# Kernel tuning notes

Hardware: AMD Instinct MI355X
Metric: run time of the kernel (lower is better)

Reference implementation:

```python
import jax, jax.numpy as jnp
import numpy as np

MIN_STD = 0.1  # cfg.min_std_dev
B, T1, S, A, H, E = 256, 128, 128, 32, 1024, 1024  # batch, T-1, state, action, belief=hidden, embedding


def setup_inputs() -> dict:
    key = jax.random.key(0)
    ks = jax.random.split(key, 16)
    f32 = jnp.float32
    def p(k, shape, fan):
        return jax.random.normal(k, shape, f32) / np.float32(np.sqrt(fan))
    return {
        "s_0": jax.random.normal(ks[0], (B, S), f32),
        "b_0": jax.random.normal(ks[1], (B, H), f32),
        "Action": jax.random.normal(ks[2], (B, T1, A), f32),
        "Observation": jax.random.normal(ks[3], (B, T1, E), f32),
        "noise_pri": jax.random.normal(ks[4], (B, T1, S), f32),
        "noise_pos": jax.random.normal(ks[5], (B, T1, S), f32),
        "W_sa": p(ks[6], (H, S + A), S + A), "b_sa": jnp.zeros((H,), f32),
        "W_ih": p(ks[7], (3 * H, H), H), "W_hh": p(ks[8], (3 * H, H), H),
        "b_ih": jnp.zeros((3 * H,), f32), "b_hh": jnp.zeros((3 * H,), f32),
        "W_bpri": p(ks[9], (H, H), H), "b_bpri": jnp.zeros((H,), f32),
        "W_spri": p(ks[10], (2 * S, H), H), "b_spri": jnp.zeros((2 * S,), f32),
        "W_bpos": p(ks[11], (H, H + E), H + E), "b_bpos": jnp.zeros((H,), f32),
        "W_spos": p(ks[12], (2 * S, H), H), "b_spos": jnp.zeros((2 * S,), f32),
    }


def reference(s_0, b_0, Action, Observation, noise_pri, noise_pos,
              W_sa, b_sa, W_ih, W_hh, b_ih, b_hh,
              W_bpri, b_bpri, W_spri, b_spri,
              W_bpos, b_bpos, W_spos, b_spos):
    act = jax.nn.relu  # cfg.activation_function = 'relu'

    def gru(x, h):  # torch.nn.GRUCell semantics, gate order r,z,n
        gi = x @ W_ih.T + b_ih
        gh = h @ W_hh.T + b_hh
        ir, iz, in_ = jnp.split(gi, 3, axis=1)
        hr, hz, hn = jnp.split(gh, 3, axis=1)
        r = jax.nn.sigmoid(ir + hr)
        z = jax.nn.sigmoid(iz + hz)
        n = jnp.tanh(in_ + r * hn)
        return (1.0 - z) * n + z * h

    def step(carry, inp):
        b, s = carry  # belief, posterior state (Observation is provided)
        a, o, ep, eq = inp
        x = act(jnp.concatenate([s, a], axis=1) @ W_sa.T + b_sa)
        b1 = gru(x, b)
        # prior
        hp = act(b1 @ W_bpri.T + b_bpri)
        mu_p, hp2 = jnp.split(hp @ W_spri.T + b_spri, 2, axis=1)
        std_p = jax.nn.softplus(hp2) + MIN_STD
        s_p = mu_p + std_p * ep
        # posterior (uses Observation[:, t])
        hq = act(jnp.concatenate([b1, o], axis=1) @ W_bpos.T + b_bpos)
        mu_q, hq2 = jnp.split(hq @ W_spos.T + b_spos, 2, axis=1)
        std_q = jax.nn.softplus(hq2) + MIN_STD
        s_q = mu_q + std_q * eq
        return (b1, s_q), (b1, s_p, mu_p, std_p, s_q, mu_q, std_q)

    xs = (jnp.swapaxes(Action, 0, 1), jnp.swapaxes(Observation, 0, 1),
          jnp.swapaxes(noise_pri, 0, 1), jnp.swapaxes(noise_pos, 0, 1))
    _, ys = jax.lax.scan(step, (b_0, s_0), xs)
    # time-major [T-1, B, D] -> batch-major [B, T-1, D]
    return tuple(jnp.swapaxes(y, 0, 1) for y in ys)
```

## Files before the change

### kernel.cpp

```cpp
#include <hip/hip_runtime.h>
#include <hip/hip_bf16.h>

typedef __hip_bfloat16 bf16;
using bf16x8 = __attribute__((ext_vector_type(8))) short;
using f32x4  = __attribute__((ext_vector_type(4))) float;

#define B_   256
#define T1_  128
#define S_   128
#define A_   32
#define H_   1024
#define E_   1024
#define MIN_STD 0.1f

__device__ __forceinline__ float loadT(const void* p, int isbf, long idx) {
  return isbf ? __bfloat162float(((const bf16*)p)[idx]) : ((const float*)p)[idx];
}
__device__ __forceinline__ void storeT(void* p, int isbf, long idx, float v) {
  if (isbf) ((bf16*)p)[idx] = __float2bfloat16(v);
  else      ((float*)p)[idx] = v;
}

__global__ void dtype_probe(const void* __restrict__ p, int nelem, int* __restrict__ flag) {
  __shared__ int bad;
  if (threadIdx.x == 0) bad = 0;
  __syncthreads();
  const bf16* q = (const bf16*)p;
  int lbad = 0;
  for (int i = threadIdx.x; i < nelem; i += 256) {
    float v = __bfloat162float(q[i]);
    if (!(fabsf(v) <= 1e6f)) lbad = 1;
  }
  if (lbad) atomicOr(&bad, 1);
  __syncthreads();
  if (threadIdx.x == 0) *flag = bad ? 0 : 1;
}

__global__ __launch_bounds__(256)
void split_plane(const void* __restrict__ src, long n, bf16* __restrict__ h,
                 bf16* __restrict__ l, const int* __restrict__ flagp) {
  const int F = *flagp;
  long i = (long)blockIdx.x * 256 + threadIdx.x;
  if (i < n) {
    float v = loadT(src, F, i);
    bf16 hv = __float2bfloat16(v);
    h[i] = hv;
    l[i] = __float2bfloat16(v - __bfloat162float(hv));
  }
}

struct GProb {
  const bf16 *Ah, *Al; int lda;
  const bf16 *A2h, *A2l; int lda2; int K1; long aoff2;
  const bf16 *Wh, *Wl; int ldw;
  const void* bias;
  float* Cf; bf16 *Ch, *Cl; int ldc;
  int relu; int nbx; int K;
};

__device__ __forceinline__ void gemm_seg(f32x4 (&acc)[2][2],
    const bf16* __restrict__ ah, const bf16* __restrict__ al, int lda, long abase,
    int ks, int ke,
    const bf16* __restrict__ wh, const bf16* __restrict__ wl, int ldw,
    int r0, int c0, int lk)
{
  #pragma unroll 2
  for (int kt = ks; kt < ke; kt += 32) {
    bf16x8 fa_h[2], fa_l[2], fw_h[2], fw_l[2];
    #pragma unroll
    for (int i = 0; i < 2; ++i) {
      long ao = (long)(r0 + i * 16) * lda + abase + (kt - ks) + lk;
      fa_h[i] = *(const bf16x8*)(ah + ao);
      fa_l[i] = *(const bf16x8*)(al + ao);
      long wo = (long)(c0 + i * 16) * ldw + kt + lk;
      fw_h[i] = *(const bf16x8*)(wh + wo);
      fw_l[i] = *(const bf16x8*)(wl + wo);
    }
    #pragma unroll
    for (int i = 0; i < 2; ++i)
      #pragma unroll
      for (int j = 0; j < 2; ++j) {
        acc[i][j] = __builtin_amdgcn_mfma_f32_16x16x32_bf16(fa_h[i], fw_h[j], acc[i][j], 0, 0, 0);
        acc[i][j] = __builtin_amdgcn_mfma_f32_16x16x32_bf16(fa_l[i], fw_h[j], acc[i][j], 0, 0, 0);
        acc[i][j] = __builtin_amdgcn_mfma_f32_16x16x32_bf16(fa_h[i], fw_l[j], acc[i][j], 0, 0, 0);
      }
  }
}

__global__ __launch_bounds__(256)
void mfma_gemm(GProb p0, GProb p1, GProb p2, int n0, int n01,
               const int* __restrict__ flagp)
{
  int blk = blockIdx.x;
  GProb p;
  if (blk < n0) p = p0;
  else if (blk < n01) { blk -= n0; p = p1; }
  else { blk -= n01; p = p2; }
  const int F = *flagp;

  const int bx   = blk % p.nbx;
  const int by   = blk / p.nbx;
  const int m0   = by * 64;
  const int nc0  = bx * 64;
  const int w    = threadIdx.x >> 6;
  const int lane = threadIdx.x & 63;
  const int wm   = (w >> 1) * 32;
  const int wn   = (w & 1) * 32;
  const int lr   = lane & 15;
  const int lk   = (lane >> 4) * 8;

  const int r0 = m0 + wm + lr;
  const int c0 = nc0 + wn + lr;

  f32x4 zz = {0.f, 0.f, 0.f, 0.f};
  f32x4 acc[2][2] = {{zz, zz}, {zz, zz}};

  gemm_seg(acc, p.Ah, p.Al, p.lda, 0, 0, p.K1, p.Wh, p.Wl, p.ldw, r0, c0, lk);
  if (p.K1 < p.K)
    gemm_seg(acc, p.A2h, p.A2l, p.lda2, p.aoff2, p.K1, p.K, p.Wh, p.Wl, p.ldw, r0, c0, lk);

  float bv0 = loadT(p.bias, F, c0);
  float bv1 = loadT(p.bias, F, c0 + 16);
  const int rb = m0 + wm + ((lane >> 4) << 2);
  #pragma unroll
  for (int i = 0; i < 2; ++i) {
    #pragma unroll
    for (int j = 0; j < 2; ++j) {
      const int n  = c0 + j * 16;
      const float bv = j ? bv1 : bv0;
      #pragma unroll
      for (int r = 0; r < 4; ++r) {
        float v = acc[i][j][r] + bv;
        if (p.relu) v = fmaxf(v, 0.f);
        long o = (long)(rb + i * 16 + r) * p.ldc + n;
        if (p.Cf) p.Cf[o] = v;
        if (p.Ch) {
          bf16 hv = __float2bfloat16(v);
          p.Ch[o] = hv;
          p.Cl[o] = __float2bfloat16(v - __bfloat162float(hv));
        }
      }
    }
  }
}

__global__ __launch_bounds__(256)
void gru_ew(const float* __restrict__ gi, const float* __restrict__ gh,
            const void* __restrict__ hprev, int hm,
            void* __restrict__ out, int t, float* __restrict__ b_f,
            bf16* __restrict__ bh, bf16* __restrict__ bl,
            const void* __restrict__ Obs, bf16* __restrict__ oh,
            bf16* __restrict__ ol, const int* __restrict__ flagp)
{
  const int F = *flagp;
  const int fh = hm & F;
  int tid = blockIdx.x * 256 + threadIdx.x;
  int b = tid >> 10;
  int j = tid & 1023;
  long gbase = (long)b * 3072;
  float ir  = gi[gbase + j],        hr = gh[gbase + j];
  float iz  = gi[gbase + 1024 + j], hz = gh[gbase + 1024 + j];
  float in_ = gi[gbase + 2048 + j], hn = gh[gbase + 2048 + j];
  float h = loadT(hprev, fh, (long)b * H_ + j);
  float r = 1.f / (1.f + expf(-(ir + hr)));
  float z = 1.f / (1.f + expf(-(iz + hz)));
  float n = tanhf(in_ + r * hn);
  float v = (1.f - z) * n + z * h;
  storeT(out, F, (long)b * (T1_ * H_) + (long)t * H_ + j, v);
  b_f[tid] = v;
  bf16 vh = __float2bfloat16(v);
  bh[tid] = vh;
  bl[tid] = __float2bfloat16(v - __bfloat162float(vh));
  float ov = loadT(Obs, F, (long)b * (T1_ * E_) + (long)t * E_ + j);
  bf16 ovh = __float2bfloat16(ov);
  oh[tid] = ovh;
  ol[tid] = __float2bfloat16(ov - __bfloat162float(ovh));
}

__device__ __forceinline__ float softplusf_(float x) {
  return fmaxf(x, 0.f) + log1pf(expf(-fabsf(x)));
}

__global__ __launch_bounds__(256)
void sample_ew(const float* __restrict__ catp, const float* __restrict__ catq,
               const void* __restrict__ npri, const void* __restrict__ npos,
               void* __restrict__ out, int t,
               bf16* __restrict__ sh, bf16* __restrict__ sl,
               const int* __restrict__ flagp)
{
  const int F = *flagp;
  int tid = blockIdx.x * 256 + threadIdx.x;
  int b = tid >> 7;
  int s = tid & 127;
  const long SZH = (long)B_ * T1_ * H_;
  const long SZS = (long)B_ * T1_ * S_;
  long nidx = (long)b * (T1_ * S_) + (long)t * S_ + s;
  long crow = (long)b * 256;
  float mu_p = catp[crow + s];
  float h2p  = catp[crow + 128 + s];
  float mu_q = catq[crow + s];
  float h2q  = catq[crow + 128 + s];
  float std_p = softplusf_(h2p) + MIN_STD;
  float std_q = softplusf_(h2q) + MIN_STD;
  float s_p = mu_p + std_p * loadT(npri, F, nidx);
  float s_q = mu_q + std_q * loadT(npos, F, nidx);
  storeT(out, F, SZH + 0 * SZS + nidx, s_p);
  storeT(out, F, SZH + 1 * SZS + nidx, mu_p);
  storeT(out, F, SZH + 2 * SZS + nidx, std_p);
  storeT(out, F, SZH + 3 * SZS + nidx, s_q);
  storeT(out, F, SZH + 4 * SZS + nidx, mu_q);
  storeT(out, F, SZH + 5 * SZS + nidx, std_q);
  bf16 qh = __float2bfloat16(s_q);
  sh[tid] = qh;
  sl[tid] = __float2bfloat16(s_q - __bfloat162float(qh));
}

extern "C" void kernel_launch(void* const* d_in, const int* in_sizes, int n_in,
                              void* d_out, int out_size, void* d_ws, size_t ws_size,
                              hipStream_t stream) {
  const void* s0     = d_in[0];
  const void* b0     = d_in[1];
  const void* Act    = d_in[2];
  const void* Obs    = d_in[3];
  const void* npri   = d_in[4];
  const void* npos   = d_in[5];
  const void* W_sa   = d_in[6];
  const void* b_sa   = d_in[7];
  const void* W_ih   = d_in[8];
  const void* W_hh   = d_in[9];
  const void* b_ih   = d_in[10];
  const void* b_hh   = d_in[11];
  const void* W_bpri = d_in[12];
  const void* b_bpri = d_in[13];
  const void* W_spri = d_in[14];
  const void* b_spri = d_in[15];
  const void* W_bpos = d_in[16];
  const void* b_bpos = d_in[17];
  const void* W_spos = d_in[18];
  const void* b_spos = d_in[19];
  (void)in_sizes; (void)n_in; (void)out_size; (void)ws_size;

  char* base = (char*)d_ws;
  size_t off = 0;
  auto carve = [&](size_t bytes) {
    void* p = base + off;
    off = (off + bytes + 255) & ~(size_t)255;
    return p;
  };
  float* gi_f   = (float*)carve(sizeof(float) * B_ * 3 * H_);
  float* gh_f   = (float*)carve(sizeof(float) * B_ * 3 * H_);
  float* b_f    = (float*)carve(sizeof(float) * B_ * H_);
  float* catp_f = (float*)carve(sizeof(float) * B_ * 2 * S_);
  float* catq_f = (float*)carve(sizeof(float) * B_ * 2 * S_);
  int*   flagp  = (int*)carve(256);
  auto plane = [&](size_t n) { return (bf16*)carve(2 * n); };
  bf16 *xh = plane((size_t)B_ * H_),  *xl = plane((size_t)B_ * H_);
  bf16 *bh = plane((size_t)B_ * H_),  *bl = plane((size_t)B_ * H_);
  bf16 *hph = plane((size_t)B_ * H_), *hpl = plane((size_t)B_ * H_);
  bf16 *hqh = plane((size_t)B_ * H_), *hql = plane((size_t)B_ * H_);
  bf16 *sh = plane((size_t)B_ * S_),  *sl = plane((size_t)B_ * S_);
  bf16 *oh = plane((size_t)B_ * E_),  *ol = plane((size_t)B_ * E_);
  bf16 *acth = plane((size_t)B_ * T1_ * A_), *actl = plane((size_t)B_ * T1_ * A_);
  bf16 *wsah  = plane((size_t)H_ * (S_ + A_)), *wsal  = plane((size_t)H_ * (S_ + A_));
  bf16 *wihh  = plane((size_t)3 * H_ * H_),    *wihl  = plane((size_t)3 * H_ * H_);
  bf16 *whhh  = plane((size_t)3 * H_ * H_),    *whhl  = plane((size_t)3 * H_ * H_);
  bf16 *wprih = plane((size_t)H_ * H_),        *wpril = plane((size_t)H_ * H_);
  bf16 *wsprih = plane((size_t)2 * S_ * H_),   *wspril = plane((size_t)2 * S_ * H_);
  bf16 *wposh = plane((size_t)H_ * (H_ + E_)), *wposl = plane((size_t)H_ * (H_ + E_));
  bf16 *wsposh = plane((size_t)2 * S_ * H_),   *wsposl = plane((size_t)2 * S_ * H_);

  dim3 blk(256);

  dtype_probe<<<dim3(1), blk, 0, stream>>>(W_ih, 8192, flagp);
  auto split = [&](const void* src, size_t n, bf16* h, bf16* l) {
    split_plane<<<dim3((unsigned)((n + 255) / 256)), blk, 0, stream>>>(src, (long)n, h, l, flagp);
  };
  split(W_sa,   (size_t)H_ * (S_ + A_), wsah, wsal);
  split(W_ih,   (size_t)3 * H_ * H_,    wihh, wihl);
  split(W_hh,   (size_t)3 * H_ * H_,    whhh, whhl);
  split(W_bpri, (size_t)H_ * H_,        wprih, wpril);
  split(W_spri, (size_t)2 * S_ * H_,    wsprih, wspril);
  split(W_bpos, (size_t)H_ * (H_ + E_), wposh, wposl);
  split(W_spos, (size_t)2 * S_ * H_,    wsposh, wsposl);
  split(s0,  (size_t)B_ * S_,        sh, sl);
  split(b0,  (size_t)B_ * H_,        bh, bl);
  split(Act, (size_t)B_ * T1_ * A_,  acth, actl);

  auto mk = [](const bf16* Ah, const bf16* Al, int lda,
               const bf16* A2h, const bf16* A2l, int lda2, int K1, long aoff2,
               const bf16* Wh, const bf16* Wl, int ldw, const void* bias,
               float* Cf, bf16* Ch, bf16* Cl, int ldc, int relu, int N, int K) {
    GProb p;
    p.Ah = Ah; p.Al = Al; p.lda = lda;
    p.A2h = A2h; p.A2l = A2l; p.lda2 = lda2; p.K1 = K1; p.aoff2 = aoff2;
    p.Wh = Wh; p.Wl = Wl; p.ldw = ldw; p.bias = bias;
    p.Cf = Cf; p.Ch = Ch; p.Cl = Cl; p.ldc = ldc;
    p.relu = relu; p.nbx = N / 64; p.K = K;
    return p;
  };

  GProb Pgh = mk(bh, bl, H_,  bh, bl, H_, H_, 0,  whhh, whhl, H_, b_hh,
                 gh_f, nullptr, nullptr, 3 * H_, 0, 3 * H_, H_);
  GProb Pgi = mk(xh, xl, H_,  xh, xl, H_, H_, 0,  wihh, wihl, H_, b_ih,
                 gi_f, nullptr, nullptr, 3 * H_, 0, 3 * H_, H_);
  GProb Px  = mk(sh, sl, S_,  acth, actl, T1_ * A_, S_, 0, wsah, wsal, S_ + A_, b_sa,
                 nullptr, xh, xl, H_, 1, H_, S_ + A_);
  GProb Php = mk(bh, bl, H_,  bh, bl, H_, H_, 0,  wprih, wpril, H_, b_bpri,
                 nullptr, hph, hpl, H_, 1, H_, H_);
  GProb Phq = mk(bh, bl, H_,  oh, ol, E_, H_, 0,  wposh, wposl, H_ + E_, b_bpos,
                 nullptr, hqh, hql, H_, 1, H_, H_ + E_);
  GProb Pcp = mk(hph, hpl, H_, hph, hpl, H_, H_, 0, wsprih, wspril, H_, b_spri,
                 catp_f, nullptr, nullptr, 2 * S_, 0, 2 * S_, H_);
  GProb Pcq = mk(hqh, hql, H_, hqh, hql, H_, H_, 0, wsposh, wsposl, H_, b_spos,
                 catq_f, nullptr, nullptr, 2 * S_, 0, 2 * S_, H_);

  mfma_gemm<<<dim3(192), blk, 0, stream>>>(Pgh, Pgh, Pgh, 192, 192, flagp);

  for (int t = 0; t < T1_; ++t) {
    Px.aoff2 = (long)t * A_;
    mfma_gemm<<<dim3(64), blk, 0, stream>>>(Px, Px, Px, 64, 64, flagp);
    mfma_gemm<<<dim3(192), blk, 0, stream>>>(Pgi, Pgi, Pgi, 192, 192, flagp);
    gru_ew<<<dim3(B_ * H_ / 256), blk, 0, stream>>>(
        gi_f, gh_f, t ? (const void*)b_f : b0, t ? 0 : 1,
        d_out, t, b_f, bh, bl, Obs, oh, ol, flagp);
    mfma_gemm<<<dim3(64 + 64 + 192), blk, 0, stream>>>(Php, Phq, Pgh, 64, 128, flagp);
    mfma_gemm<<<dim3(32), blk, 0, stream>>>(Pcp, Pcq, Pcq, 16, 32, flagp);
    sample_ew<<<dim3(B_ * S_ / 256), blk, 0, stream>>>(
        catp_f, catq_f, npri, npos, d_out, t, sh, sl, flagp);
  }
}
```

Measured before the change: 21.27 ms.

## Fuse recurrent time loop into one persistent kernel with grid barriers

Replaces the per-timestep sequence of six kernel launches with a single persistent 256-block kernel that walks all timesteps, separating phases with a custom atomic grid barrier. GEMM tiles grow from 64x64 to 128x128 per block. The observation half of the posterior GEMM is computed off the critical path, alongside the input-gate GEMM. The posterior sample is rebuilt inside the x-projection tile instead of being staged through bf16 planes. This removes roughly 768 launches and their gaps, at the cost of fewer active blocks per GEMM and a grid barrier that deadlocks unless all 256 blocks are co-resident.

```diff
diff --git a/kernel.cpp b/kernel.cpp
--- a/kernel.cpp
+++ b/kernel.cpp
@@ -12,6 +12,8 @@
 #define H_   1024
 #define E_   1024
 #define MIN_STD 0.1f
+#define GRID_ 256
+#define ASTRIDE 16
 
 __device__ __forceinline__ float loadT(const void* p, int isbf, long idx) {
   return isbf ? __bfloat162float(((const bf16*)p)[idx]) : ((const float*)p)[idx];
@@ -20,8 +22,15 @@
   if (isbf) ((bf16*)p)[idx] = __float2bfloat16(v);
   else      ((float*)p)[idx] = v;
 }
-
-__global__ void dtype_probe(const void* __restrict__ p, int nelem, int* __restrict__ flag) {
+__device__ __forceinline__ float softplusf_(float x) {
+  return fmaxf(x, 0.f) + log1pf(expf(-fabsf(x)));
+}
+__device__ __forceinline__ short f2bf_s(float v) {
+  union { bf16 b; short s; } u; u.b = __float2bfloat16(v); return u.s;
+}
+
+__global__ void dtype_probe(const void* __restrict__ p, int nelem, int* __restrict__ flag,
+                            int* __restrict__ arrive, int* __restrict__ phasep) {
   __shared__ int bad;
   if (threadIdx.x == 0) bad = 0;
   __syncthreads();
@@ -32,8 +41,9 @@
     if (!(fabsf(v) <= 1e6f)) lbad = 1;
   }
   if (lbad) atomicOr(&bad, 1);
+  for (int i = threadIdx.x; i < GRID_ * ASTRIDE; i += 256) arrive[i] = 0;
   __syncthreads();
-  if (threadIdx.x == 0) *flag = bad ? 0 : 1;
+  if (threadIdx.x == 0) { *flag = bad ? 0 : 1; *phasep = 0; }
 }
 
 __global__ __launch_bounds__(256)
@@ -49,170 +59,319 @@
   }
 }
 
-struct GProb {
-  const bf16 *Ah, *Al; int lda;
-  const bf16 *A2h, *A2l; int lda2; int K1; long aoff2;
-  const bf16 *Wh, *Wl; int ldw;
-  const void* bias;
-  float* Cf; bf16 *Ch, *Cl; int ldc;
-  int relu; int nbx; int K;
+__device__ __forceinline__ void gbar(int* arrive, int* phasep, int epoch) {
+  __syncthreads();
+  if (blockIdx.x == 0) {
+    if (threadIdx.x > 0) {
+      int* a = arrive + threadIdx.x * ASTRIDE;
+      while (__hip_atomic_load(a, __ATOMIC_RELAXED, __HIP_MEMORY_SCOPE_AGENT) < epoch)
+        __builtin_amdgcn_s_sleep(1);
+    }
+    __threadfence();
+    __syncthreads();
+    if (threadIdx.x == 0)
+      __hip_atomic_store(phasep, epoch, __ATOMIC_RELEASE, __HIP_MEMORY_SCOPE_AGENT);
+  } else {
+    if (threadIdx.x == 0) {
+      __threadfence();
+      __hip_atomic_store(arrive + blockIdx.x * ASTRIDE, epoch,
+                         __ATOMIC_RELEASE, __HIP_MEMORY_SCOPE_AGENT);
+      while (__hip_atomic_load(phasep, __ATOMIC_RELAXED, __HIP_MEMORY_SCOPE_AGENT) < epoch)
+        __builtin_amdgcn_s_sleep(1);
+      __threadfence();
+    }
+    __syncthreads();
+  }
+}
+
+struct KP {
+  const void *s0, *b0, *Act, *Obs, *npri, *npos;
+  const void *b_sa, *b_ih, *b_hh, *b_bpri, *b_spri, *b_bpos, *b_spos;
+  void* out;
+  float *gi_f, *gh_f, *b_f, *catp_f, *catq_f, *hqo_f;
+  bf16 *xh, *xl, *bh, *bl, *hph, *hpl, *hqh, *hql, *oh, *ol, *acth, *actl;
+  const bf16 *wsah, *wsal, *wihh, *wihl, *whhh, *whhl;
+  const bf16 *wprih, *wpril, *wsprih, *wspril, *wposh, *wposl, *wsposh, *wsposl;
+  const int* flagp;
+  int *arrive, *phasep;
 };
 
-__device__ __forceinline__ void gemm_seg(f32x4 (&acc)[2][2],
-    const bf16* __restrict__ ah, const bf16* __restrict__ al, int lda, long abase,
-    int ks, int ke,
-    const bf16* __restrict__ wh, const bf16* __restrict__ wl, int ldw,
-    int r0, int c0, int lk)
+struct GArg {
+  const bf16 *ah, *al; int lda;
+  const bf16 *wh, *wl; int ldw; int wbase;
+  const void* bias; const float* cadd;
+  float* cf; bf16 *ch; bf16 *cl; int ldc;
+  int relu; int K; int nbx;
+};
+
+__device__ __forceinline__ void mfma3(f32x4& a, bf16x8 ah, bf16x8 al, bf16x8 wh, bf16x8 wl) {
+  a = __builtin_amdgcn_mfma_f32_16x16x32_bf16(ah, wh, a, 0, 0, 0);
+  a = __builtin_amdgcn_mfma_f32_16x16x32_bf16(al, wh, a, 0, 0, 0);
+  a = __builtin_amdgcn_mfma_f32_16x16x32_bf16(ah, wl, a, 0, 0, 0);
+}
+
+__device__ __forceinline__ void epilogue(f32x4 (&acc)[4][4], int m0, int n0, int wm, int wn,
+    int lane, int F, const void* bias, const float* cadd,
+    float* cf, bf16* ch, bf16* cl, int ldc, int relu)
 {
-  #pragma unroll 2
-  for (int kt = ks; kt < ke; kt += 32) {
-    bf16x8 fa_h[2], fa_l[2], fw_h[2], fw_l[2];
-    #pragma unroll
-    for (int i = 0; i < 2; ++i) {
-      long ao = (long)(r0 + i * 16) * lda + abase + (kt - ks) + lk;
-      fa_h[i] = *(const bf16x8*)(ah + ao);
-      fa_l[i] = *(const bf16x8*)(al + ao);
-      long wo = (long)(c0 + i * 16) * ldw + kt + lk;
-      fw_h[i] = *(const bf16x8*)(wh + wo);
-      fw_l[i] = *(const bf16x8*)(wl + wo);
-    }
-    #pragma unroll
-    for (int i = 0; i < 2; ++i)
-      #pragma unroll
-      for (int j = 0; j < 2; ++j) {
-        acc[i][j] = __builtin_amdgcn_mfma_f32_16x16x32_bf16(fa_h[i], fw_h[j], acc[i][j], 0, 0, 0);
-        acc[i][j] = __builtin_amdgcn_mfma_f32_16x16x32_bf16(fa_l[i], fw_h[j], acc[i][j], 0, 0, 0);
-        acc[i][j] = __builtin_amdgcn_mfma_f32_16x16x32_bf16(fa_h[i], fw_l[j], acc[i][j], 0, 0, 0);
-      }
-  }
-}
-
-__global__ __launch_bounds__(256)
-void mfma_gemm(GProb p0, GProb p1, GProb p2, int n0, int n01,
-               const int* __restrict__ flagp)
-{
-  int blk = blockIdx.x;
-  GProb p;
-  if (blk < n0) p = p0;
-  else if (blk < n01) { blk -= n0; p = p1; }
-  else { blk -= n01; p = p2; }
-  const int F = *flagp;
-
-  const int bx   = blk % p.nbx;
-  const int by   = blk / p.nbx;
-  const int m0   = by * 64;
-  const int nc0  = bx * 64;
-  const int w    = threadIdx.x >> 6;
-  const int lane = threadIdx.x & 63;
-  const int wm   = (w >> 1) * 32;
-  const int wn   = (w & 1) * 32;
-  const int lr   = lane & 15;
-  const int lk   = (lane >> 4) * 8;
-
-  const int r0 = m0 + wm + lr;
-  const int c0 = nc0 + wn + lr;
-
-  f32x4 zz = {0.f, 0.f, 0.f, 0.f};
-  f32x4 acc[2][2] = {{zz, zz}, {zz, zz}};
-
-  gemm_seg(acc, p.Ah, p.Al, p.lda, 0, 0, p.K1, p.Wh, p.Wl, p.ldw, r0, c0, lk);
-  if (p.K1 < p.K)
-    gemm_seg(acc, p.A2h, p.A2l, p.lda2, p.aoff2, p.K1, p.K, p.Wh, p.Wl, p.ldw, r0, c0, lk);
-
-  float bv0 = loadT(p.bias, F, c0);
-  float bv1 = loadT(p.bias, F, c0 + 16);
+  const int lr = lane & 15;
   const int rb = m0 + wm + ((lane >> 4) << 2);
   #pragma unroll
-  for (int i = 0; i < 2; ++i) {
-    #pragma unroll
-    for (int j = 0; j < 2; ++j) {
-      const int n  = c0 + j * 16;
-      const float bv = j ? bv1 : bv0;
+  for (int j = 0; j < 4; ++j) {
+    const int n = n0 + wn + 16 * j + lr;
+    const float bv = bias ? loadT(bias, F, n) : 0.f;
+    #pragma unroll
+    for (int i = 0; i < 4; ++i) {
       #pragma unroll
       for (int r = 0; r < 4; ++r) {
+        long o = (long)(rb + 16 * i + r) * ldc + n;
         float v = acc[i][j][r] + bv;
-        if (p.relu) v = fmaxf(v, 0.f);
-        long o = (long)(rb + i * 16 + r) * p.ldc + n;
-        if (p.Cf) p.Cf[o] = v;
-        if (p.Ch) {
-          bf16 hv = __float2bfloat16(v);
-          p.Ch[o] = hv;
-          p.Cl[o] = __float2bfloat16(v - __bfloat162float(hv));
+        if (cadd) v += cadd[o];
+        if (relu) v = fmaxf(v, 0.f);
+        if (cf) cf[o] = v;
+        if (ch) {
+          bf16 hb = __float2bfloat16(v);
+          ch[o] = hb;
+          cl[o] = __float2bfloat16(v - __bfloat162float(hb));
         }
       }
     }
   }
 }
 
-__global__ __launch_bounds__(256)
-void gru_ew(const float* __restrict__ gi, const float* __restrict__ gh,
-            const void* __restrict__ hprev, int hm,
-            void* __restrict__ out, int t, float* __restrict__ b_f,
-            bf16* __restrict__ bh, bf16* __restrict__ bl,
-            const void* __restrict__ Obs, bf16* __restrict__ oh,
-            bf16* __restrict__ ol, const int* __restrict__ flagp)
-{
-  const int F = *flagp;
-  const int fh = hm & F;
-  int tid = blockIdx.x * 256 + threadIdx.x;
-  int b = tid >> 10;
-  int j = tid & 1023;
-  long gbase = (long)b * 3072;
-  float ir  = gi[gbase + j],        hr = gh[gbase + j];
-  float iz  = gi[gbase + 1024 + j], hz = gh[gbase + 1024 + j];
-  float in_ = gi[gbase + 2048 + j], hn = gh[gbase + 2048 + j];
-  float h = loadT(hprev, fh, (long)b * H_ + j);
+__device__ void run_gemm(const GArg& g, int tile, int F, int wm, int wn, int lr, int lk8, int lane) {
+  const int m0 = (tile / g.nbx) * 128;
+  const int n0 = (tile % g.nbx) * 128;
+  const int r0 = m0 + wm + lr;
+  const int c0 = n0 + wn + lr;
+  f32x4 acc[4][4];
+  #pragma unroll
+  for (int i = 0; i < 4; ++i)
+    #pragma unroll
+    for (int j = 0; j < 4; ++j) acc[i][j] = (f32x4){0.f, 0.f, 0.f, 0.f};
+
+  #pragma unroll 2
+  for (int kt = 0; kt < g.K; kt += 32) {
+    bf16x8 fah[4], fal[4], fwh[4], fwl[4];
+    #pragma unroll
+    for (int i = 0; i < 4; ++i) {
+      long ao = (long)(r0 + 16 * i) * g.lda + kt + lk8;
+      fah[i] = *(const bf16x8*)(g.ah + ao);
+      fal[i] = *(const bf16x8*)(g.al + ao);
+    }
+    #pragma unroll
+    for (int j = 0; j < 4; ++j) {
+      long wo = (long)(c0 + 16 * j) * g.ldw + g.wbase + kt + lk8;
+      fwh[j] = *(const bf16x8*)(g.wh + wo);
+      fwl[j] = *(const bf16x8*)(g.wl + wo);
+    }
+    #pragma unroll
+    for (int i = 0; i < 4; ++i)
+      #pragma unroll
+      for (int j = 0; j < 4; ++j)
+        mfma3(acc[i][j], fah[i], fal[i], fwh[j], fwl[j]);
+  }
+  epilogue(acc, m0, n0, wm, wn, lane, F, g.bias, g.cadd, g.cf, g.ch, g.cl, g.ldc, g.relu);
+}
+
+__device__ void x_tile(const KP& p, int F, int t, int tile, int wm, int wn, int lr, int lk8, int lane) {
+  const int m0 = (tile / 8) * 128;
+  const int n0 = (tile % 8) * 128;
+  const int r0 = m0 + wm + lr;
+  const int c0 = n0 + wn + lr;
+  f32x4 acc[4][4];
+  #pragma unroll
+  for (int i = 0; i < 4; ++i)
+    #pragma unroll
+    for (int j = 0; j < 4; ++j) acc[i][j] = (f32x4){0.f, 0.f, 0.f, 0.f};
+
+  for (int kt = 0; kt < 128; kt += 32) {
+    bf16x8 fah[4], fal[4], fwh[4], fwl[4];
+    #pragma unroll
+    for (int i = 0; i < 4; ++i) {
+      const int r = r0 + 16 * i;
+      const int k0 = kt + lk8;
+      #pragma unroll
+      for (int e = 0; e < 8; ++e) {
+        const int kk = k0 + e;
+        float v;
+        if (t == 0) {
+          v = loadT(p.s0, F, (long)r * S_ + kk);
+        } else {
+          float mu  = p.catq_f[(long)r * 256 + kk];
+          float h2  = p.catq_f[(long)r * 256 + 128 + kk];
+          float eps = loadT(p.npos, F, (long)r * (T1_ * S_) + (long)(t - 1) * S_ + kk);
+          v = mu + (softplusf_(h2) + MIN_STD) * eps;
+        }
+        bf16 hb = __float2bfloat16(v);
+        union { bf16 b; short s; } u; u.b = hb;
+        fah[i][e] = u.s;
+        fal[i][e] = f2bf_s(v - __bfloat162float(hb));
+      }
+    }
+    #pragma unroll
+    for (int j = 0; j < 4; ++j) {
+      long wo = (long)(c0 + 16 * j) * (S_ + A_) + kt + lk8;
+      fwh[j] = *(const bf16x8*)(p.wsah + wo);
+      fwl[j] = *(const bf16x8*)(p.wsal + wo);
+    }
+    #pragma unroll
+    for (int i = 0; i < 4; ++i)
+      #pragma unroll
+      for (int j = 0; j < 4; ++j)
+        mfma3(acc[i][j], fah[i], fal[i], fwh[j], fwl[j]);
+  }
+  {
+    bf16x8 fah[4], fal[4], fwh[4], fwl[4];
+    #pragma unroll
+    for (int i = 0; i < 4; ++i) {
+      long ao = (long)(r0 + 16 * i) * (T1_ * A_) + (long)t * A_ + lk8;
+      fah[i] = *(const bf16x8*)(p.acth + ao);
+      fal[i] = *(const bf16x8*)(p.actl + ao);
+    }
+    #pragma unroll
+    for (int j = 0; j < 4; ++j) {
+      long wo = (long)(c0 + 16 * j) * (S_ + A_) + 128 + lk8;
+      fwh[j] = *(const bf16x8*)(p.wsah + wo);
+      fwl[j] = *(const bf16x8*)(p.wsal + wo);
+    }
+    #pragma unroll
+    for (int i = 0; i < 4; ++i)
+      #pragma unroll
+      for (int j = 0; j < 4; ++j)
+        mfma3(acc[i][j], fah[i], fal[i], fwh[j], fwl[j]);
+  }
+  epilogue(acc, m0, n0, wm, wn, lane, F, p.b_sa, nullptr, nullptr, p.xh, p.xl, H_, 1);
+}
+
+__device__ __forceinline__ void gru_elem(const KP& p, int F, int t, int idx) {
+  int b = idx >> 10, j = idx & 1023;
+  long g3 = (long)b * 3072;
+  float ir  = p.gi_f[g3 + j],        hr = p.gh_f[g3 + j];
+  float iz  = p.gi_f[g3 + 1024 + j], hz = p.gh_f[g3 + 1024 + j];
+  float in_ = p.gi_f[g3 + 2048 + j], hn = p.gh_f[g3 + 2048 + j];
+  float h = t ? p.b_f[idx] : loadT(p.b0, F, idx);
   float r = 1.f / (1.f + expf(-(ir + hr)));
   float z = 1.f / (1.f + expf(-(iz + hz)));
   float n = tanhf(in_ + r * hn);
   float v = (1.f - z) * n + z * h;
-  storeT(out, F, (long)b * (T1_ * H_) + (long)t * H_ + j, v);
-  b_f[tid] = v;
-  bf16 vh = __float2bfloat16(v);
-  bh[tid] = vh;
-  bl[tid] = __float2bfloat16(v - __bfloat162float(vh));
-  float ov = loadT(Obs, F, (long)b * (T1_ * E_) + (long)t * E_ + j);
-  bf16 ovh = __float2bfloat16(ov);
-  oh[tid] = ovh;
-  ol[tid] = __float2bfloat16(ov - __bfloat162float(ovh));
-}
-
-__device__ __forceinline__ float softplusf_(float x) {
-  return fmaxf(x, 0.f) + log1pf(expf(-fabsf(x)));
-}
-
-__global__ __launch_bounds__(256)
-void sample_ew(const float* __restrict__ catp, const float* __restrict__ catq,
-               const void* __restrict__ npri, const void* __restrict__ npos,
-               void* __restrict__ out, int t,
-               bf16* __restrict__ sh, bf16* __restrict__ sl,
-               const int* __restrict__ flagp)
-{
-  const int F = *flagp;
-  int tid = blockIdx.x * 256 + threadIdx.x;
-  int b = tid >> 7;
-  int s = tid & 127;
+  storeT(p.out, F, (long)b * (T1_ * H_) + (long)t * H_ + j, v);
+  p.b_f[idx] = v;
+  bf16 hb = __float2bfloat16(v);
+  p.bh[idx] = hb;
+  p.bl[idx] = __float2bfloat16(v - __bfloat162float(hb));
+}
+
+__device__ __forceinline__ void sample_elem(const KP& p, int F, int t, int idx) {
+  int b = idx >> 7, s = idx & 127;
   const long SZH = (long)B_ * T1_ * H_;
   const long SZS = (long)B_ * T1_ * S_;
   long nidx = (long)b * (T1_ * S_) + (long)t * S_ + s;
   long crow = (long)b * 256;
-  float mu_p = catp[crow + s];
-  float h2p  = catp[crow + 128 + s];
-  float mu_q = catq[crow + s];
-  float h2q  = catq[crow + 128 + s];
+  float mu_p = p.catp_f[crow + s];
+  float h2p  = p.catp_f[crow + 128 + s];
+  float mu_q = p.catq_f[crow + s];
+  float h2q  = p.catq_f[crow + 128 + s];
   float std_p = softplusf_(h2p) + MIN_STD;
   float std_q = softplusf_(h2q) + MIN_STD;
-  float s_p = mu_p + std_p * loadT(npri, F, nidx);
-  float s_q = mu_q + std_q * loadT(npos, F, nidx);
-  storeT(out, F, SZH + 0 * SZS + nidx, s_p);
-  storeT(out, F, SZH + 1 * SZS + nidx, mu_p);
-  storeT(out, F, SZH + 2 * SZS + nidx, std_p);
-  storeT(out, F, SZH + 3 * SZS + nidx, s_q);
-  storeT(out, F, SZH + 4 * SZS + nidx, mu_q);
-  storeT(out, F, SZH + 5 * SZS + nidx, std_q);
-  bf16 qh = __float2bfloat16(s_q);
-  sh[tid] = qh;
-  sl[tid] = __float2bfloat16(s_q - __bfloat162float(qh));
+  float s_p = mu_p + std_p * loadT(p.npri, F, nidx);
+  float s_q = mu_q + std_q * loadT(p.npos, F, nidx);
+  storeT(p.out, F, SZH + 0 * SZS + nidx, s_p);
+  storeT(p.out, F, SZH + 1 * SZS + nidx, mu_p);
+  storeT(p.out, F, SZH + 2 * SZS + nidx, std_p);
+  storeT(p.out, F, SZH + 3 * SZS + nidx, s_q);
+  storeT(p.out, F, SZH + 4 * SZS + nidx, mu_q);
+  storeT(p.out, F, SZH + 5 * SZS + nidx, std_q);
+}
+
+__global__ __launch_bounds__(256, 1) void fused_seq(KP p) {
+  const int F    = *p.flagp;
+  const int blk  = blockIdx.x;
+  const int tid  = threadIdx.x;
+  const int w    = tid >> 6;
+  const int lane = tid & 63;
+  const int wm   = (w >> 1) * 64;
+  const int wn   = (w & 1) * 64;
+  const int lr   = lane & 15;
+  const int lk8  = (lane >> 4) * 8;
+
+  int epoch = 0;
+  #define GSYNC() gbar(p.arrive, p.phasep, ++epoch)
+
+  {
+    GArg g = { p.bh, p.bl, H_, p.whhh, p.whhl, H_, 0, p.b_hh, nullptr,
+               p.gh_f, nullptr, nullptr, 3 * H_, 0, H_, 24 };
+    if (blk < 48) run_gemm(g, blk, F, wm, wn, lr, lk8, lane);
+  }
+  GSYNC();
+
+  for (int t = 0; t < T1_; ++t) {
+    if (blk < 16) {
+      x_tile(p, F, t, blk, wm, wn, lr, lk8, lane);
+    } else if (blk < 240) {
+      int pos = (blk - 16) * 256 + tid;
+      for (int i = pos; i < B_ * E_; i += 224 * 256) {
+        int b = i >> 10, j = i & 1023;
+        float ov = loadT(p.Obs, F, (long)b * (T1_ * E_) + (long)t * E_ + j);
+        bf16 hb = __float2bfloat16(ov);
+        p.oh[i] = hb;
+        p.ol[i] = __float2bfloat16(ov - __bfloat162float(hb));
+      }
+    } else if (t > 0) {
+      int pos = (blk - 240) * 256 + tid;
+      for (int i = pos; i < B_ * S_; i += 4096) sample_elem(p, F, t - 1, i);
+    }
+    GSYNC();
+
+    if (blk < 48) {
+      GArg g = { p.xh, p.xl, H_, p.wihh, p.wihl, H_, 0, p.b_ih, nullptr,
+                 p.gi_f, nullptr, nullptr, 3 * H_, 0, H_, 24 };
+      run_gemm(g, blk, F, wm, wn, lr, lk8, lane);
+    } else if (blk < 64) {
+      GArg g = { p.oh, p.ol, E_, p.wposh, p.wposl, H_ + E_, H_, p.b_bpos, nullptr,
+                 p.hqo_f, nullptr, nullptr, H_, 0, H_, 8 };
+      run_gemm(g, blk - 48, F, wm, wn, lr, lk8, lane);
+    }
+    GSYNC();
+
+    {
+      int pos = blk * 256 + tid;
+      for (int i = pos; i < B_ * H_; i += GRID_ * 256) gru_elem(p, F, t, i);
+    }
+    GSYNC();
+
+    if (blk < 16) {
+      GArg g = { p.bh, p.bl, H_, p.wprih, p.wpril, H_, 0, p.b_bpri, nullptr,
+                 nullptr, p.hph, p.hpl, H_, 1, H_, 8 };
+      run_gemm(g, blk, F, wm, wn, lr, lk8, lane);
+    } else if (blk < 32) {
+      GArg g = { p.bh, p.bl, H_, p.wposh, p.wposl, H_ + E_, 0, nullptr, p.hqo_f,
+                 nullptr, p.hqh, p.hql, H_, 1, H_, 8 };
+      run_gemm(g, blk - 16, F, wm, wn, lr, lk8, lane);
+    } else if (blk < 80) {
+      GArg g = { p.bh, p.bl, H_, p.whhh, p.whhl, H_, 0, p.b_hh, nullptr,
+                 p.gh_f, nullptr, nullptr, 3 * H_, 0, H_, 24 };
+      run_gemm(g, blk - 32, F, wm, wn, lr, lk8, lane);
+    }
+    GSYNC();
+
+    if (blk < 4) {
+      GArg g = { p.hph, p.hpl, H_, p.wsprih, p.wspril, H_, 0, p.b_spri, nullptr,
+                 p.catp_f, nullptr, nullptr, 2 * S_, 0, H_, 2 };
+      run_gemm(g, blk, F, wm, wn, lr, lk8, lane);
+    } else if (blk < 8) {
+      GArg g = { p.hqh, p.hql, H_, p.wsposh, p.wsposl, H_, 0, p.b_spos, nullptr,
+                 p.catq_f, nullptr, nullptr, 2 * S_, 0, H_, 2 };
+      run_gemm(g, blk - 4, F, wm, wn, lr, lk8, lane);
+    }
+    GSYNC();
+  }
+
+  {
+    int pos = blk * 256 + tid;
+    if (pos < B_ * S_) sample_elem(p, F, T1_ - 1, pos);
+  }
+  #undef GSYNC
 }
 
 extern "C" void kernel_launch(void* const* d_in, const int* in_sizes, int n_in,
@@ -243,22 +402,24 @@
   char* base = (char*)d_ws;
   size_t off = 0;
   auto carve = [&](size_t bytes) {
-    void* p = base + off;
+    void* q = base + off;
     off = (off + bytes + 255) & ~(size_t)255;
-    return p;
+    return q;
   };
   float* gi_f   = (float*)carve(sizeof(float) * B_ * 3 * H_);
   float* gh_f   = (float*)carve(sizeof(float) * B_ * 3 * H_);
   float* b_f    = (float*)carve(sizeof(float) * B_ * H_);
   float* catp_f = (float*)carve(sizeof(float) * B_ * 2 * S_);
   float* catq_f = (float*)carve(sizeof(float) * B_ * 2 * S_);
+  float* hqo_f  = (float*)carve(sizeof(float) * B_ * H_);
   int*   flagp  = (int*)carve(256);
+  int*   arrive = (int*)carve(sizeof(int) * GRID_ * ASTRIDE);
+  int*   phasep = (int*)carve(256);
   auto plane = [&](size_t n) { return (bf16*)carve(2 * n); };
   bf16 *xh = plane((size_t)B_ * H_),  *xl = plane((size_t)B_ * H_);
   bf16 *bh = plane((size_t)B_ * H_),  *bl = plane((size_t)B_ * H_);
   bf16 *hph = plane((size_t)B_ * H_), *hpl = plane((size_t)B_ * H_);
   bf16 *hqh = plane((size_t)B_ * H_), *hql = plane((size_t)B_ * H_);
-  bf16 *sh = plane((size_t)B_ * S_),  *sl = plane((size_t)B_ * S_);
   bf16 *oh = plane((size_t)B_ * E_),  *ol = plane((size_t)B_ * E_);
   bf16 *acth = plane((size_t)B_ * T1_ * A_), *actl = plane((size_t)B_ * T1_ * A_);
   bf16 *wsah  = plane((size_t)H_ * (S_ + A_)), *wsal  = plane((size_t)H_ * (S_ + A_));
@@ -271,7 +432,7 @@
 
   dim3 blk(256);
 
-  dtype_probe<<<dim3(1), blk, 0, stream>>>(W_ih, 8192, flagp);
+  dtype_probe<<<dim3(1), blk, 0, stream>>>(W_ih, 8192, flagp, arrive, phasep);
   auto split = [&](const void* src, size_t n, bf16* h, bf16* l) {
     split_plane<<<dim3((unsigned)((n + 255) / 256)), blk, 0, stream>>>(src, (long)n, h, l, flagp);
   };
@@ -282,50 +443,25 @@
   split(W_spri, (size_t)2 * S_ * H_,    wsprih, wspril);
   split(W_bpos, (size_t)H_ * (H_ + E_), wposh, wposl);
   split(W_spos, (size_t)2 * S_ * H_,    wsposh, wsposl);
-  split(s0,  (size_t)B_ * S_,        sh, sl);
-  split(b0,  (size_t)B_ * H_,        bh, bl);
-  split(Act, (size_t)B_ * T1_ * A_,  acth, actl);
-
-  auto mk = [](const bf16* Ah, const bf16* Al, int lda,
-               const bf16* A2h, const bf16* A2l, int lda2, int K1, long aoff2,
-               const bf16* Wh, const bf16* Wl, int ldw, const void* bias,
-               float* Cf, bf16* Ch, bf16* Cl, int ldc, int relu, int N, int K) {
-    GProb p;
-    p.Ah = Ah; p.Al = Al; p.lda = lda;
-    p.A2h = A2h; p.A2l = A2l; p.lda2 = lda2; p.K1 = K1; p.aoff2 = aoff2;
-    p.Wh = Wh; p.Wl = Wl; p.ldw = ldw; p.bias = bias;
-    p.Cf = Cf; p.Ch = Ch; p.Cl = Cl; p.ldc = ldc;
-    p.relu = relu; p.nbx = N / 64; p.K = K;
-    return p;
-  };
-
-  GProb Pgh = mk(bh, bl, H_,  bh, bl, H_, H_, 0,  whhh, whhl, H_, b_hh,
-                 gh_f, nullptr, nullptr, 3 * H_, 0, 3 * H_, H_);
-  GProb Pgi = mk(xh, xl, H_,  xh, xl, H_, H_, 0,  wihh, wihl, H_, b_ih,
-                 gi_f, nullptr, nullptr, 3 * H_, 0, 3 * H_, H_);
-  GProb Px  = mk(sh, sl, S_,  acth, actl, T1_ * A_, S_, 0, wsah, wsal, S_ + A_, b_sa,
-                 nullptr, xh, xl, H_, 1, H_, S_ + A_);
-  GProb Php = mk(bh, bl, H_,  bh, bl, H_, H_, 0,  wprih, wpril, H_, b_bpri,
-                 nullptr, hph, hpl, H_, 1, H_, H_);
-  GProb Phq = mk(bh, bl, H_,  oh, ol, E_, H_, 0,  wposh, wposl, H_ + E_, b_bpos,
-                 nullptr, hqh, hql, H_, 1, H_, H_ + E_);
-  GProb Pcp = mk(hph, hpl, H_, hph, hpl, H_, H_, 0, wsprih, wspril, H_, b_spri,
-                 catp_f, nullptr, nullptr, 2 * S_, 0, 2 * S_, H_);
-  GProb Pcq = mk(hqh, hql, H_, hqh, hql, H_, H_, 0, wsposh, wsposl, H_, b_spos,
-                 catq_f, nullptr, nullptr, 2 * S_, 0, 2 * S_, H_);
-
-  mfma_gemm<<<dim3(192), blk, 0, stream>>>(Pgh, Pgh, Pgh, 192, 192, flagp);
-
-  for (int t = 0; t < T1_; ++t) {
-    Px.aoff2 = (long)t * A_;
-    mfma_gemm<<<dim3(64), blk, 0, stream>>>(Px, Px, Px, 64, 64, flagp);
-    mfma_gemm<<<dim3(192), blk, 0, stream>>>(Pgi, Pgi, Pgi, 192, 192, flagp);
-    gru_ew<<<dim3(B_ * H_ / 256), blk, 0, stream>>>(
-        gi_f, gh_f, t ? (const void*)b_f : b0, t ? 0 : 1,
-        d_out, t, b_f, bh, bl, Obs, oh, ol, flagp);
-    mfma_gemm<<<dim3(64 + 64 + 192), blk, 0, stream>>>(Php, Phq, Pgh, 64, 128, flagp);
-    mfma_gemm<<<dim3(32), blk, 0, stream>>>(Pcp, Pcq, Pcq, 16, 32, flagp);
-    sample_ew<<<dim3(B_ * S_ / 256), blk, 0, stream>>>(
-        catp_f, catq_f, npri, npos, d_out, t, sh, sl, flagp);
-  }
-}
+  split(b0,  (size_t)B_ * H_,           bh, bl);
+  split(Act, (size_t)B_ * T1_ * A_,     acth, actl);
+
+  KP kp;
+  kp.s0 = s0; kp.b0 = b0; kp.Act = Act; kp.Obs = Obs; kp.npri = npri; kp.npos = npos;
+  kp.b_sa = b_sa; kp.b_ih = b_ih; kp.b_hh = b_hh; kp.b_bpri = b_bpri;
+  kp.b_spri = b_spri; kp.b_bpos = b_bpos; kp.b_spos = b_spos;
+  kp.out = d_out;
+  kp.gi_f = gi_f; kp.gh_f = gh_f; kp.b_f = b_f;
+  kp.catp_f = catp_f; kp.catq_f = catq_f; kp.hqo_f = hqo_f;
+  kp.xh = xh; kp.xl = xl; kp.bh = bh; kp.bl = bl;
+  kp.hph = hph; kp.hpl = hpl; kp.hqh = hqh; kp.hql = hql;
+  kp.oh = oh; kp.ol = ol; kp.acth = acth; kp.actl = actl;
+  kp.wsah = wsah; kp.wsal = wsal; kp.wihh = wihh; kp.wihl = wihl;
+  kp.whhh = whhh; kp.whhl = whhl; kp.wprih = wprih; kp.wpril = wpril;
+  kp.wsprih = wsprih; kp.wspril = wspril; kp.wposh = wposh; kp.wposl = wposl;
+  kp.wsposh = wsposh; kp.wsposl = wsposl;
+  kp.flagp = flagp;
+  kp.arrive = arrive; kp.phasep = phasep;
+
+  fused_seq<<<dim3(GRID_), blk, 0, stream>>>(kp);
+}
```

Result: slower. 47.42 ms (+123.0%).
